# Performance work log

Measured on AMD Instinct MI355X. Metric: run time of the kernel, lower is better.

## Reference

```python
import jax, jax.numpy as jnp
import numpy as np

ALPHA = 2.0  # ATan surrogate alpha (spikingjelly default)
V_TH = 1.0   # v_threshold
H = 8        # num_heads

@jax.custom_vjp
def atan_spike(x):
    # heaviside(v - v_th); x = v - v_th
    return (x >= 0.0).astype(x.dtype)

def _spike_fwd(x):
    return atan_spike(x), x

def _spike_bwd(x, g):
    pi_half = jnp.asarray(np.pi / 2, x.dtype)
    grad = (ALPHA / 2.0) / (1.0 + (pi_half * ALPHA * x) ** 2)
    return (g * grad,)

atan_spike.defvjp(_spike_fwd, _spike_bwd)

def lif(x_seq, w):
    # MultiStepParametricLIFNode: recurrence over leading dim of x_seq.
    # v <- v + (x - (v - v_reset)) * sigmoid(w); v_reset = 0; hard reset, detach_reset=True.
    sg = jax.nn.sigmoid(w)
    def step(v, x):
        h = v + (x - v) * sg
        s = atan_spike(h - V_TH)
        v_new = h * (1.0 - jax.lax.stop_gradient(s))  # hard reset to 0, detached spike
        return v_new, s
    v0 = jnp.zeros_like(x_seq[0])
    _, spikes = jax.lax.scan(step, v0, x_seq)
    return spikes


def setup_inputs() -> dict:
    key = jax.random.key(0)
    ks = jax.random.split(key, 6)
    T, B, N, C = 4, 32, 196, 512
    s = 0.02
    return {
        "x": jax.random.normal(ks[0], (T, B, N, C), dtype=jnp.float32),
        "Wq": jax.random.normal(ks[1], (C, C), dtype=jnp.float32) * s,
        "Wk": jax.random.normal(ks[2], (C, C), dtype=jnp.float32) * s,
        "Wv": jax.random.normal(ks[3], (C, C), dtype=jnp.float32) * s,
        "Wp": jax.random.normal(ks[4], (C, C), dtype=jnp.float32) * s,
        "bp": jax.random.normal(ks[5], (C,), dtype=jnp.float32) * s,
        "wq": jnp.zeros((), jnp.float32),  # init_tau=2 -> w=0
        "wk": jnp.zeros((), jnp.float32),
        "wv": jnp.zeros((), jnp.float32),
        "wa": jnp.zeros((), jnp.float32),
        "wp": jnp.zeros((), jnp.float32),
    }


def reference(x, Wq, Wk, Wv, Wp, bp, wq, wk, wv, wa, wp):
    T, B, N, C = x.shape
    d = C // H
    scale = d ** (-0.5)
    xf = x.reshape(T * B, N, C)  # LIF steps over T*B (faithful to original flatten(0,1))

    def qkv(W, w_lif):
        y = lif(xf @ W.T, w_lif)                       # [T*B, N, C] binary spikes
        return y.reshape(T, B, N, H, d).transpose(0, 1, 3, 2, 4)  # [T,B,H,N,d]

    q = qkv(Wq, wq)
    k = qkv(Wk, wk)
    v = qkv(Wv, wv)

    attn = jnp.einsum('tbhnd,tbhmd->tbhnm', q, k) * scale   # softmax-free
    y = jnp.einsum('tbhnm,tbhmd->tbhnd', attn, v)           # [T,B,H,N,d]
    y = y.swapaxes(3, 4).reshape(T, B, N, C)                # faithful transpose(3,4).reshape

    y = lif(y, wa)                                          # attn_lif steps over T
    out = lif(y.reshape(T * B, N, C) @ Wp.T + bp, wp)       # proj_lif steps over T*B
    return out.reshape(T, B, N, C)
```

## Files before the change

### kernel.cpp

```cpp
#include <hip/hip_runtime.h>

#define NC 100352
typedef unsigned long long ull;

template <int NMAT, bool BIAS>
__global__ __launch_bounds__(256) void gemm16(
    const float* __restrict__ A,
    const float* __restrict__ W0, const float* __restrict__ W1,
    const float* __restrict__ W2, const float* __restrict__ bias,
    float* __restrict__ C0, float* __restrict__ C1, float* __restrict__ C2)
{
    __shared__ float As[16][260];
    __shared__ float Bs[16][132];

    const int chunk = (NMAT * 392) >> 3;
    const int w = ((int)blockIdx.x & 7) * chunk + ((int)blockIdx.x >> 3);
    const int rp = w / (4 * NMAT);
    const int rem = w - rp * (4 * NMAT);
    const int br = rem >> 2;
    const int cb = rem & 3;

    const float* Wb = (NMAT == 1 || br == 0) ? W0 : (br == 1 ? W1 : W2);
    float* Cb = (NMAT == 1 || br == 0) ? C0 : (br == 1 ? C1 : C2);

    const int tid = threadIdx.x;
    const int r0 = tid >> 2;
    const int kq = (tid & 3) << 2;
    const int rg = (tid >> 4) << 2;
    const int cg = (tid & 15) << 2;

    float acc[16][8] = {};
    const float* Ap = A + (size_t)(rp * 256 + r0) * 512 + kq;
    const float* Bp = Wb + (size_t)(cb * 128 + r0) * 512 + kq;

    for (int k0 = 0; k0 < 512; k0 += 16) {
        float4 a[4], b[2];
#pragma unroll
        for (int s = 0; s < 4; ++s)
            a[s] = *(const float4*)(Ap + (size_t)s * 64 * 512 + k0);
#pragma unroll
        for (int s = 0; s < 2; ++s)
            b[s] = *(const float4*)(Bp + (size_t)s * 64 * 512 + k0);
        __syncthreads();
#pragma unroll
        for (int s = 0; s < 4; ++s) {
            As[kq + 0][r0 + s * 64] = a[s].x;
            As[kq + 1][r0 + s * 64] = a[s].y;
            As[kq + 2][r0 + s * 64] = a[s].z;
            As[kq + 3][r0 + s * 64] = a[s].w;
        }
#pragma unroll
        for (int s = 0; s < 2; ++s) {
            Bs[kq + 0][r0 + s * 64] = b[s].x;
            Bs[kq + 1][r0 + s * 64] = b[s].y;
            Bs[kq + 2][r0 + s * 64] = b[s].z;
            Bs[kq + 3][r0 + s * 64] = b[s].w;
        }
        __syncthreads();
#pragma unroll
        for (int k = 0; k < 16; ++k) {
            float av[16], bv[8];
#pragma unroll
            for (int s = 0; s < 4; ++s)
                *(float4*)&av[s * 4] = *(const float4*)&As[k][rg + s * 64];
#pragma unroll
            for (int s = 0; s < 2; ++s)
                *(float4*)&bv[s * 4] = *(const float4*)&Bs[k][cg + s * 64];
#pragma unroll
            for (int i = 0; i < 16; ++i)
#pragma unroll
                for (int j = 0; j < 8; ++j)
                    acc[i][j] = fmaf(av[i], bv[j], acc[i][j]);
        }
    }

#pragma unroll
    for (int s = 0; s < 4; ++s)
#pragma unroll
        for (int i = 0; i < 4; ++i) {
            const int row = rp * 256 + s * 64 + rg + i;
#pragma unroll
            for (int jh = 0; jh < 2; ++jh) {
                const int col = cb * 128 + cg + jh * 64;
                float4 o;
                o.x = acc[s * 4 + i][jh * 4 + 0];
                o.y = acc[s * 4 + i][jh * 4 + 1];
                o.z = acc[s * 4 + i][jh * 4 + 2];
                o.w = acc[s * 4 + i][jh * 4 + 3];
                if (BIAS) {
                    o.x += bias[col + 0]; o.y += bias[col + 1];
                    o.z += bias[col + 2]; o.w += bias[col + 3];
                }
                *(float4*)&Cb[(size_t)row * 512 + col] = o;
            }
        }
}

template <int NMAT, bool BIAS>
__global__ __launch_bounds__(256) void gemm_nt(
    const float* __restrict__ A,
    const float* __restrict__ W0, const float* __restrict__ W1,
    const float* __restrict__ W2, const float* __restrict__ bias,
    float* __restrict__ C0, float* __restrict__ C1, float* __restrict__ C2)
{
    __shared__ float As[16][132];
    __shared__ float Bs[16][132];

    const int chunk = (NMAT * 784) >> 3;
    const int w = ((int)blockIdx.x & 7) * chunk + ((int)blockIdx.x >> 3);
    const int rp = w / (4 * NMAT);
    const int rem = w - rp * (4 * NMAT);
    const int br = rem >> 2;
    const int cb = rem & 3;

    const float* Wb = (NMAT == 1 || br == 0) ? W0 : (br == 1 ? W1 : W2);
    float* Cb = (NMAT == 1 || br == 0) ? C0 : (br == 1 ? C1 : C2);

    const int tid = threadIdx.x;
    const int r0 = tid >> 2;
    const int kq = (tid & 3) << 2;
    const int rg = (tid >> 4) << 2;
    const int cg = (tid & 15) << 2;

    float acc[8][8] = {};
    const float* A0 = A + (size_t)(rp * 128 + r0) * 512 + kq;
    const float* A1 = A0 + (size_t)64 * 512;
    const float* B0 = Wb + (size_t)(cb * 128 + r0) * 512 + kq;
    const float* B1 = B0 + (size_t)64 * 512;

    for (int k0 = 0; k0 < 512; k0 += 16) {
        const float4 a0 = *(const float4*)(A0 + k0);
        const float4 a1 = *(const float4*)(A1 + k0);
        const float4 b0 = *(const float4*)(B0 + k0);
        const float4 b1 = *(const float4*)(B1 + k0);
        __syncthreads();
        As[kq + 0][r0] = a0.x; As[kq + 1][r0] = a0.y; As[kq + 2][r0] = a0.z; As[kq + 3][r0] = a0.w;
        As[kq + 0][r0 + 64] = a1.x; As[kq + 1][r0 + 64] = a1.y; As[kq + 2][r0 + 64] = a1.z; As[kq + 3][r0 + 64] = a1.w;
        Bs[kq + 0][r0] = b0.x; Bs[kq + 1][r0] = b0.y; Bs[kq + 2][r0] = b0.z; Bs[kq + 3][r0] = b0.w;
        Bs[kq + 0][r0 + 64] = b1.x; Bs[kq + 1][r0 + 64] = b1.y; Bs[kq + 2][r0 + 64] = b1.z; Bs[kq + 3][r0 + 64] = b1.w;
        __syncthreads();
#pragma unroll
        for (int k = 0; k < 16; ++k) {
            float av[8], bv[8];
            *(float4*)&av[0] = *(const float4*)&As[k][rg];
            *(float4*)&av[4] = *(const float4*)&As[k][rg + 64];
            *(float4*)&bv[0] = *(const float4*)&Bs[k][cg];
            *(float4*)&bv[4] = *(const float4*)&Bs[k][cg + 64];
#pragma unroll
            for (int i = 0; i < 8; ++i)
#pragma unroll
                for (int j = 0; j < 8; ++j)
                    acc[i][j] = fmaf(av[i], bv[j], acc[i][j]);
        }
    }

#pragma unroll
    for (int ih = 0; ih < 2; ++ih)
#pragma unroll
        for (int i = 0; i < 4; ++i) {
            const int row = rp * 128 + rg + i + ih * 64;
#pragma unroll
            for (int jh = 0; jh < 2; ++jh) {
                const int col = cb * 128 + cg + jh * 64;
                float4 o;
                o.x = acc[ih * 4 + i][jh * 4 + 0];
                o.y = acc[ih * 4 + i][jh * 4 + 1];
                o.z = acc[ih * 4 + i][jh * 4 + 2];
                o.w = acc[ih * 4 + i][jh * 4 + 3];
                if (BIAS) {
                    o.x += bias[col + 0]; o.y += bias[col + 1];
                    o.z += bias[col + 2]; o.w += bias[col + 3];
                }
                *(float4*)&Cb[(size_t)row * 512 + col] = o;
            }
        }
}

__global__ __launch_bounds__(256) void lif_mask3(
    const float* __restrict__ U0, const float* __restrict__ U1,
    const float* __restrict__ U2,
    const float* __restrict__ wq, const float* __restrict__ wk,
    const float* __restrict__ wv, ull* __restrict__ M)
{
    const int br = blockIdx.x / 392;
    const int blk = blockIdx.x - br * 392;
    const int i = blk * 256 + threadIdx.x;
    const float* U = (br == 0) ? U0 : (br == 1 ? U1 : U2);
    const float wv_ = (br == 0) ? wq[0] : (br == 1 ? wk[0] : wv[0]);
    const float sg = 1.0f / (1.0f + expf(-wv_));
    ull* Mw = M + (size_t)br * 200704 + ((i >> 6) & 7) * 196 + (i >> 9);
    float v = 0.0f;
    for (int t = 0; t < 128; ++t) {
        const float x = U[(size_t)t * NC + i];
        const float h = __fadd_rn(v, __fmul_rn(__fsub_rn(x, v), sg));
        const bool sp = (h >= 1.0f);
        const ull m = __ballot(sp);
        if ((threadIdx.x & 63) == 0) Mw[(size_t)t * 1568] = m;
        v = sp ? 0.0f : h;
    }
}

__global__ __launch_bounds__(256) void lif_out(const float* __restrict__ U,
                                               const float* __restrict__ wp,
                                               float* __restrict__ out)
{
    const int i = blockIdx.x * 256 + threadIdx.x;
    const float sg = 1.0f / (1.0f + expf(-wp[0]));
    float v = 0.0f;
    for (int t = 0; t < 128; ++t) {
        const float x = U[(size_t)t * NC + i];
        const float h = __fadd_rn(v, __fmul_rn(__fsub_rn(x, v), sg));
        const bool sp = (h >= 1.0f);
        out[(size_t)t * NC + i] = sp ? 1.0f : 0.0f;
        v = sp ? 0.0f : h;
    }
}

__global__ __launch_bounds__(256) void attn_fused(const ull* __restrict__ Qm,
                                                  const ull* __restrict__ Km,
                                                  const ull* __restrict__ Vm,
                                                  const float* __restrict__ wa,
                                                  float* __restrict__ Y)
{
    const int b = blockIdx.x >> 3;
    const int h = blockIdx.x & 7;
    const int tid = threadIdx.x;
    const int w = tid >> 6;
    const int lane = tid & 63;

    __shared__ ull qrow[256], krow[256], vrow[256];
    __shared__ ull kcol[64][5], vcol[64][5];
    __shared__ ushort G[64][64];
    __shared__ float vstate[196][64];
    __shared__ ull sbm[208];

    const float sg = 1.0f / (1.0f + expf(-wa[0]));

    for (int t = 0; t < 4; ++t) {
        const int tb = t * 32 + b;
        const size_t mb = (size_t)tb * 1568 + (size_t)h * 196;
        if (tid < 196) {
            qrow[tid] = Qm[mb + tid];
            krow[tid] = Km[mb + tid];
            vrow[tid] = Vm[mb + tid];
        } else {
            qrow[tid] = 0; krow[tid] = 0; vrow[tid] = 0;
        }
        __syncthreads();

        {
            ull kc = 0, vc = 0;
#pragma unroll 8
            for (int m = 0; m < 64; ++m) {
                kc |= ((krow[w * 64 + m] >> lane) & 1ull) << m;
                vc |= ((vrow[w * 64 + m] >> lane) & 1ull) << m;
            }
            kcol[lane][w] = kc; vcol[lane][w] = vc;
        }
        __syncthreads();

        for (int p = tid; p < 4096; p += 256) {
            const int d1 = p >> 6, d2 = p & 63;
            const int g = __popcll(kcol[d1][0] & vcol[d2][0]) +
                          __popcll(kcol[d1][1] & vcol[d2][1]) +
                          __popcll(kcol[d1][2] & vcol[d2][2]) +
                          __popcll(kcol[d1][3] & vcol[d2][3]);
            G[d1][d2] = (ushort)g;
        }
        __syncthreads();

        {
            int r = 49 * w;
            const int rend = r + 49;
            for (; r + 1 < rend; r += 2) {
                const ull q0 = qrow[r], q1 = qrow[r + 1];
                const uint a0 = (uint)q0, a1 = (uint)(q0 >> 32);
                const uint b0 = (uint)q1, b1 = (uint)(q1 >> 32);
                uint s0 = 0, s1 = 0;
#pragma unroll
                for (int d = 0; d < 32; ++d) {
                    const uint g = G[d][lane];
                    s0 += ((a0 >> d) & 1u) * g;
                    s1 += ((b0 >> d) & 1u) * g;
                }
#pragma unroll
                for (int d = 0; d < 32; ++d) {
                    const uint g = G[32 + d][lane];
                    s0 += ((a1 >> d) & 1u) * g;
                    s1 += ((b1 >> d) & 1u) * g;
                }
                const float y0 = (float)s0 * 0.125f;
                const float v0 = t ? vstate[r][lane] : 0.0f;
                const float h0 = __fadd_rn(v0, __fmul_rn(__fsub_rn(y0, v0), sg));
                const bool sp0 = h0 >= 1.0f;
                vstate[r][lane] = sp0 ? 0.0f : h0;
                const ull m0 = __ballot(sp0);
                const float y1 = (float)s1 * 0.125f;
                const float v1 = t ? vstate[r + 1][lane] : 0.0f;
                const float h1 = __fadd_rn(v1, __fmul_rn(__fsub_rn(y1, v1), sg));
                const bool sp1 = h1 >= 1.0f;
                vstate[r + 1][lane] = sp1 ? 0.0f : h1;
                const ull m1 = __ballot(sp1);
                if (lane == 0) { sbm[r] = m0; sbm[r + 1] = m1; }
            }
            {
                const ull q0 = qrow[r];
                const uint a0 = (uint)q0, a1 = (uint)(q0 >> 32);
                uint s0 = 0;
#pragma unroll
                for (int d = 0; d < 32; ++d) s0 += ((a0 >> d) & 1u) * (uint)G[d][lane];
#pragma unroll
                for (int d = 0; d < 32; ++d) s0 += ((a1 >> d) & 1u) * (uint)G[32 + d][lane];
                const float y0 = (float)s0 * 0.125f;
                const float v0 = t ? vstate[r][lane] : 0.0f;
                const float h0 = __fadd_rn(v0, __fmul_rn(__fsub_rn(y0, v0), sg));
                const bool sp0 = h0 >= 1.0f;
                vstate[r][lane] = sp0 ? 0.0f : h0;
                const ull m0 = __ballot(sp0);
                if (lane == 0) sbm[r] = m0;
            }
        }
        __syncthreads();

        const size_t yb = (size_t)tb * NC + (size_t)h * 12544;
        for (int f = tid; f < 12544; f += 256) {
            const int e = f / 196;
            const int r2 = f - e * 196;
            Y[yb + f] = ((sbm[r2] >> e) & 1ull) ? 1.0f : 0.0f;
        }
        __syncthreads();
    }
}

extern "C" void kernel_launch(void* const* d_in, const int* in_sizes, int n_in,
                              void* d_out, int out_size, void* d_ws, size_t ws_size,
                              hipStream_t stream) {
    const float* x  = (const float*)d_in[0];
    const float* Wq = (const float*)d_in[1];
    const float* Wk = (const float*)d_in[2];
    const float* Wv = (const float*)d_in[3];
    const float* Wp = (const float*)d_in[4];
    const float* bp = (const float*)d_in[5];
    const float* wq = (const float*)d_in[6];
    const float* wk = (const float*)d_in[7];
    const float* wv = (const float*)d_in[8];
    const float* wa = (const float*)d_in[9];
    const float* wp = (const float*)d_in[10];
    float* out = (float*)d_out;

    char* ws = (char*)d_ws;
    float* u0 = (float*)ws;
    float* u1 = (float*)(ws + (size_t)51380224);
    float* u2 = (float*)(ws + (size_t)2 * 51380224);
    ull* Qm   = (ull*)(ws + (size_t)3 * 51380224);
    ull* Km   = Qm + 200704;
    ull* Vm   = Km + 200704;
    float* ySc = u0;
    float* up  = u1;

    gemm16<3, false><<<1176, 256, 0, stream>>>(x, Wq, Wk, Wv, nullptr,
                                               u0, u1, u2);
    lif_mask3<<<1176, 256, 0, stream>>>(u0, u1, u2, wq, wk, wv, Qm);

    attn_fused<<<256, 256, 0, stream>>>(Qm, Km, Vm, wa, ySc);

    gemm_nt<1, true><<<784, 256, 0, stream>>>(ySc, Wp, nullptr, nullptr, bp,
                                              up, nullptr, nullptr);
    lif_out<<<392, 256, 0, stream>>>(up, wp, out);
}
```

Measured before the change: 860.9 us.

## Pack attention spikes as bitmask and decode them inside projection GEMM

The attention kernel now writes its binary spike output as packed 32-bit bitmasks instead of a full float tensor. The projection GEMM is replaced by a kernel that reads those bits directly and expands them to 0/1 floats in registers, which drops the A-operand shared-memory staging. This removes a large float write and re-read of the spike tensor, at the cost of bit-extraction ALU work and scattered per-row mask loads. Separately, the QKV GEMM gets a launch bound of one block per SM, which changes its register budget.

```diff
diff --git a/kernel.cpp b/kernel.cpp
--- a/kernel.cpp
+++ b/kernel.cpp
@@ -4,7 +4,7 @@
 typedef unsigned long long ull;
 
 template <int NMAT, bool BIAS>
-__global__ __launch_bounds__(256) void gemm16(
+__global__ __launch_bounds__(256, 1) void gemm16(
     const float* __restrict__ A,
     const float* __restrict__ W0, const float* __restrict__ W1,
     const float* __restrict__ W2, const float* __restrict__ bias,
@@ -96,25 +96,16 @@
         }
 }
 
-template <int NMAT, bool BIAS>
-__global__ __launch_bounds__(256) void gemm_nt(
-    const float* __restrict__ A,
-    const float* __restrict__ W0, const float* __restrict__ W1,
-    const float* __restrict__ W2, const float* __restrict__ bias,
-    float* __restrict__ C0, float* __restrict__ C1, float* __restrict__ C2)
-{
-    __shared__ float As[16][132];
+__global__ __launch_bounds__(256) void gemm_mask(
+    const uint* __restrict__ Am,
+    const float* __restrict__ W, const float* __restrict__ bias,
+    float* __restrict__ C)
+{
     __shared__ float Bs[16][132];
 
-    const int chunk = (NMAT * 784) >> 3;
-    const int w = ((int)blockIdx.x & 7) * chunk + ((int)blockIdx.x >> 3);
-    const int rp = w / (4 * NMAT);
-    const int rem = w - rp * (4 * NMAT);
-    const int br = rem >> 2;
-    const int cb = rem & 3;
-
-    const float* Wb = (NMAT == 1 || br == 0) ? W0 : (br == 1 ? W1 : W2);
-    float* Cb = (NMAT == 1 || br == 0) ? C0 : (br == 1 ? C1 : C2);
+    const int w = ((int)blockIdx.x & 7) * 98 + ((int)blockIdx.x >> 3);
+    const int rp = w >> 2;
+    const int cb = w & 3;
 
     const int tid = threadIdx.x;
     const int r0 = tid >> 2;
@@ -122,30 +113,44 @@
     const int rg = (tid >> 4) << 2;
     const int cg = (tid & 15) << 2;
 
+    const float* B0 = W + (size_t)(cb * 128 + r0) * 512 + kq;
+    const float* B1 = B0 + (size_t)64 * 512;
+
+    const uint* mp[8];
+#pragma unroll
+    for (int ih = 0; ih < 2; ++ih)
+#pragma unroll
+        for (int i = 0; i < 4; ++i) {
+            const int row = rp * 128 + rg + i + ih * 64;
+            const int tb = row / 196;
+            const int n = row - tb * 196;
+            mp[ih * 4 + i] = Am + (size_t)tb * 3136 + n * 16;
+        }
+
     float acc[8][8] = {};
-    const float* A0 = A + (size_t)(rp * 128 + r0) * 512 + kq;
-    const float* A1 = A0 + (size_t)64 * 512;
-    const float* B0 = Wb + (size_t)(cb * 128 + r0) * 512 + kq;
-    const float* B1 = B0 + (size_t)64 * 512;
 
     for (int k0 = 0; k0 < 512; k0 += 16) {
-        const float4 a0 = *(const float4*)(A0 + k0);
-        const float4 a1 = *(const float4*)(A1 + k0);
         const float4 b0 = *(const float4*)(B0 + k0);
         const float4 b1 = *(const float4*)(B1 + k0);
-        __syncthreads();
-        As[kq + 0][r0] = a0.x; As[kq + 1][r0] = a0.y; As[kq + 2][r0] = a0.z; As[kq + 3][r0] = a0.w;
-        As[kq + 0][r0 + 64] = a1.x; As[kq + 1][r0 + 64] = a1.y; As[kq + 2][r0 + 64] = a1.z; As[kq + 3][r0 + 64] = a1.w;
-        Bs[kq + 0][r0] = b0.x; Bs[kq + 1][r0] = b0.y; Bs[kq + 2][r0] = b0.z; Bs[kq + 3][r0] = b0.w;
-        Bs[kq + 0][r0 + 64] = b1.x; Bs[kq + 1][r0 + 64] = b1.y; Bs[kq + 2][r0 + 64] = b1.z; Bs[kq + 3][r0 + 64] = b1.w;
+        uint wv[8];
+        const int wi = k0 >> 5;
+        const int sh = k0 & 16;
+#pragma unroll
+        for (int m = 0; m < 8; ++m) wv[m] = mp[m][wi] >> sh;
+        __syncthreads();
+        Bs[kq + 0][r0] = b0.x; Bs[kq + 1][r0] = b0.y;
+        Bs[kq + 2][r0] = b0.z; Bs[kq + 3][r0] = b0.w;
+        Bs[kq + 0][r0 + 64] = b1.x; Bs[kq + 1][r0 + 64] = b1.y;
+        Bs[kq + 2][r0 + 64] = b1.z; Bs[kq + 3][r0 + 64] = b1.w;
         __syncthreads();
 #pragma unroll
         for (int k = 0; k < 16; ++k) {
-            float av[8], bv[8];
-            *(float4*)&av[0] = *(const float4*)&As[k][rg];
-            *(float4*)&av[4] = *(const float4*)&As[k][rg + 64];
+            float bv[8], av[8];
             *(float4*)&bv[0] = *(const float4*)&Bs[k][cg];
             *(float4*)&bv[4] = *(const float4*)&Bs[k][cg + 64];
+#pragma unroll
+            for (int m = 0; m < 8; ++m)
+                av[m] = ((wv[m] >> k) & 1u) ? 1.0f : 0.0f;
 #pragma unroll
             for (int i = 0; i < 8; ++i)
 #pragma unroll
@@ -163,15 +168,11 @@
             for (int jh = 0; jh < 2; ++jh) {
                 const int col = cb * 128 + cg + jh * 64;
                 float4 o;
-                o.x = acc[ih * 4 + i][jh * 4 + 0];
-                o.y = acc[ih * 4 + i][jh * 4 + 1];
-                o.z = acc[ih * 4 + i][jh * 4 + 2];
-                o.w = acc[ih * 4 + i][jh * 4 + 3];
-                if (BIAS) {
-                    o.x += bias[col + 0]; o.y += bias[col + 1];
-                    o.z += bias[col + 2]; o.w += bias[col + 3];
-                }
-                *(float4*)&Cb[(size_t)row * 512 + col] = o;
+                o.x = acc[ih * 4 + i][jh * 4 + 0] + bias[col + 0];
+                o.y = acc[ih * 4 + i][jh * 4 + 1] + bias[col + 1];
+                o.z = acc[ih * 4 + i][jh * 4 + 2] + bias[col + 2];
+                o.w = acc[ih * 4 + i][jh * 4 + 3] + bias[col + 3];
+                *(float4*)&C[(size_t)row * 512 + col] = o;
             }
         }
 }
@@ -220,7 +221,7 @@
                                                   const ull* __restrict__ Km,
                                                   const ull* __restrict__ Vm,
                                                   const float* __restrict__ wa,
-                                                  float* __restrict__ Y)
+                                                  uint* __restrict__ Ym)
 {
     const int b = blockIdx.x >> 3;
     const int h = blockIdx.x & 7;
@@ -322,11 +323,20 @@
         }
         __syncthreads();
 
-        const size_t yb = (size_t)tb * NC + (size_t)h * 12544;
-        for (int f = tid; f < 12544; f += 256) {
-            const int e = f / 196;
-            const int r2 = f - e * 196;
-            Y[yb + f] = ((sbm[r2] >> e) & 1ull) ? 1.0f : 0.0f;
+        {
+            uint* Yw = Ym + (size_t)tb * 3136 + h * 392;
+            for (int wd = tid; wd < 392; wd += 256) {
+                const int fb = wd * 32;
+                const int e0 = fb / 196;
+                const int r0 = fb - e0 * 196;
+                const int run = (196 - r0 >= 32) ? 32 : (196 - r0);
+                uint word = 0;
+                for (int j = 0; j < run; ++j)
+                    word |= (uint)((sbm[r0 + j] >> e0) & 1ull) << j;
+                for (int j = run; j < 32; ++j)
+                    word |= (uint)((sbm[j - run] >> (e0 + 1)) & 1ull) << j;
+                Yw[wd] = word;
+            }
         }
         __syncthreads();
     }
@@ -355,16 +365,16 @@
     ull* Qm   = (ull*)(ws + (size_t)3 * 51380224);
     ull* Km   = Qm + 200704;
     ull* Vm   = Km + 200704;
-    float* ySc = u0;
-    float* up  = u1;
+    uint* Ym  = (uint*)(ws + (size_t)3 * 51380224 + (size_t)3 * 1605632);
+    float* up = u0;
 
     gemm16<3, false><<<1176, 256, 0, stream>>>(x, Wq, Wk, Wv, nullptr,
                                                u0, u1, u2);
     lif_mask3<<<1176, 256, 0, stream>>>(u0, u1, u2, wq, wk, wv, Qm);
 
-    attn_fused<<<256, 256, 0, stream>>>(Qm, Km, Vm, wa, ySc);
-
-    gemm_nt<1, true><<<784, 256, 0, stream>>>(ySc, Wp, nullptr, nullptr, bp,
-                                              up, nullptr, nullptr);
+    attn_fused<<<256, 256, 0, stream>>>(Qm, Km, Vm, wa, Ym);
+
+    gemm_mask<<<784, 256, 0, stream>>>(Ym, Wp, bp, up);
+
     lif_out<<<392, 256, 0, stream>>>(up, wp, out);
 }
```

After: 924.8 us. 1.07x slower.
